# Kernel tuning notes

Measured on AMD Instinct MI355X. Metric: run time of the kernel, lower is better.

Reference implementation:

```python
import jax, jax.numpy as jnp
import numpy as np
import math

B, T, C = 2, 2048, 768
NH, HD = 12, 64  # n_head, head_dim

def setup_inputs() -> dict:
    key = jax.random.key(0)
    k1, k2, k3 = jax.random.split(key, 3)
    x = jax.random.normal(k1, (B, T, C), dtype=jnp.float32)
    mask = jnp.tril(jnp.ones((T, T), dtype=bool))[None, None]  # [1,1,T,T] causal
    Wqkv = jax.random.normal(k2, (C, 3 * C), dtype=jnp.float32) * (1.0 / math.sqrt(C))
    Wproj = jax.random.normal(k3, (C, C), dtype=jnp.float32) * (1.0 / math.sqrt(C))
    return {"x": x, "mask": mask, "Wqkv": Wqkv, "Wproj": Wproj}

def reference(x, mask, Wqkv, Wproj):
    b, t, c = x.shape
    qkv = x @ Wqkv  # [b,t,3c]
    q, k, v = jnp.split(qkv, 3, axis=-1)
    q = q.reshape(b, t, NH, HD).transpose(0, 2, 1, 3)  # [b,h,t,d]
    k = k.reshape(b, t, NH, HD).transpose(0, 2, 1, 3)
    v = v.reshape(b, t, NH, HD).transpose(0, 2, 1, 3)
    att = jnp.einsum('bhqd,bhkd->bhqk', q, k) / math.sqrt(HD)
    att = jnp.where(mask, att, -jnp.inf)
    att = jax.nn.softmax(att, axis=-1)
    out = jnp.einsum('bhqk,bhkd->bhqd', att, v)
    out = out.transpose(0, 2, 1, 3).reshape(b, t, c)
    return out @ Wproj
```

## Files before the change

### kernel.cpp

```cpp
#include <hip/hip_runtime.h>
#include <hip/hip_bf16.h>

#define T_   2048
#define C_   768
#define NH_  12
#define HD_  64
#define M_   (2*T_)
#define N1_  (3*C_)
#define PB_  ((size_t)NH_*T_*HD_)
#define KS_  0.180336880f

typedef __attribute__((ext_vector_type(8))) short  short8;
typedef __attribute__((ext_vector_type(4))) float  floatx4;

__device__ __forceinline__ floatx4 mfma_bf16(short8 a, short8 b, floatx4 c) {
    return __builtin_amdgcn_mfma_f32_16x16x32_bf16(a, b, c, 0, 0, 0);
}

__device__ __forceinline__ float fast_exp2(float x) {
    return __builtin_amdgcn_exp2f(x);
}

#define XSZ  3145728
#define WQSZ 1769472
#define WPSZ 589824
__global__ __launch_bounds__(256) void prep_cvt(const float* __restrict__ x,
                                                const float* __restrict__ wqkv,
                                                const float* __restrict__ wproj,
                                                __hip_bfloat16* __restrict__ xb,
                                                __hip_bfloat16* __restrict__ wqkvT,
                                                __hip_bfloat16* __restrict__ wprojT) {
    const int idx = blockIdx.x * 256 + threadIdx.x;
    if (idx < XSZ) {
        xb[idx] = __float2bfloat16(x[idx]);
    } else if (idx < XSZ + WQSZ) {
        const int j = idx - XSZ;
        const int n = j / C_, k = j - n * C_;
        wqkvT[j] = __float2bfloat16(wqkv[(size_t)k * N1_ + n]);
    } else {
        const int j = idx - XSZ - WQSZ;
        const int n = j / C_, k = j - n * C_;
        wprojT[j] = __float2bfloat16(wproj[(size_t)k * C_ + n]);
    }
}

__global__ __launch_bounds__(256) void gemm_bt(const __hip_bfloat16* __restrict__ A,
                                               const __hip_bfloat16* __restrict__ Bt,
                                               int N, int K, int mode,
                                               void* __restrict__ O0,
                                               __hip_bfloat16* __restrict__ O1,
                                               __hip_bfloat16* __restrict__ O2) {
    __shared__ __align__(16) __hip_bfloat16 As[64 * 40];
    __shared__ __align__(16) __hip_bfloat16 Bs[64 * 40];

    const int tid  = threadIdx.x;
    const int n0   = blockIdx.x * 64;
    const int m0   = blockIdx.y * 64;
    const int srow = tid >> 2;
    const int scol = (tid & 3) * 8;
    const int wave = tid >> 6;
    const int ln   = tid & 63;
    const int l16  = ln & 15;
    const int q4   = ln >> 4;
    const int wm   = (wave >> 1) * 32;
    const int wn   = (wave & 1) * 32;

    floatx4 acc[2][2];
#pragma unroll
    for (int i = 0; i < 2; i++)
#pragma unroll
        for (int j = 0; j < 2; j++) acc[i][j] = (floatx4){0.f, 0.f, 0.f, 0.f};

    const __hip_bfloat16* Ap = A  + (size_t)(m0 + srow) * K + scol;
    const __hip_bfloat16* Bp = Bt + (size_t)(n0 + srow) * K + scol;

    for (int k0 = 0; k0 < K; k0 += 32) {
        short8 av = *(const short8*)(Ap + k0);
        short8 bv = *(const short8*)(Bp + k0);
        __syncthreads();
        *(short8*)(As + srow * 40 + scol) = av;
        *(short8*)(Bs + srow * 40 + scol) = bv;
        __syncthreads();
        short8 af[2], bfr[2];
#pragma unroll
        for (int i = 0; i < 2; i++) {
            af[i]  = *(const short8*)(As + (wm + i * 16 + l16) * 40 + q4 * 8);
            bfr[i] = *(const short8*)(Bs + (wn + i * 16 + l16) * 40 + q4 * 8);
        }
#pragma unroll
        for (int i = 0; i < 2; i++)
#pragma unroll
            for (int j = 0; j < 2; j++)
                acc[i][j] = mfma_bf16(af[i], bfr[j], acc[i][j]);
    }

#pragma unroll
    for (int i = 0; i < 2; i++) {
        const int mbase = m0 + wm + i * 16 + q4 * 4;
#pragma unroll
        for (int j = 0; j < 2; j++) {
            const int n = n0 + wn + j * 16 + l16;
#pragma unroll
            for (int r = 0; r < 4; r++) {
                const int mm = mbase + r;
                const float fv = acc[i][j][r];
                if (mode == 1) {
                    ((float*)O0)[(size_t)mm * N + n] = fv;
                } else {
                    const __hip_bfloat16 hv = __float2bfloat16(fv);
                    const int which = n / C_;
                    const int rem   = n - which * C_;
                    const int h     = rem >> 6;
                    const int d     = rem & 63;
                    const int bh    = (mm >> 11) * NH_ + h;
                    const int t     = mm & (T_ - 1);
                    if (which == 0)      ((__hip_bfloat16*)O0)[((size_t)bh * T_ + t) * HD_ + d] = hv;
                    else if (which == 1) O1[((size_t)bh * T_ + t) * HD_ + d] = hv;
                    else                 O2[((size_t)bh * HD_ + d) * T_ + t] = hv;
                }
            }
        }
    }
}

__global__ __launch_bounds__(256) void gemm_xw(const void* __restrict__ A,
                                               const float* __restrict__ Bf,
                                               int a_is_f32, int row0, int N, int K,
                                               int mode, int orow0,
                                               void* __restrict__ O0,
                                               __hip_bfloat16* __restrict__ O1,
                                               __hip_bfloat16* __restrict__ O2) {
    __shared__ __align__(16) __hip_bfloat16 As[64 * 40];
    __shared__ __align__(16) __hip_bfloat16 Bs[64 * 40];

    const int tid  = threadIdx.x;
    const int n0   = blockIdx.x * 64;
    const int m0   = blockIdx.y * 64;
    const int srow = tid >> 2;
    const int scol = (tid & 3) * 8;
    const int wave = tid >> 6;
    const int ln   = tid & 63;
    const int l16  = ln & 15;
    const int q4   = ln >> 4;
    const int wm   = (wave >> 1) * 32;
    const int wn   = (wave & 1) * 32;

    floatx4 acc[2][2];
#pragma unroll
    for (int i = 0; i < 2; i++)
#pragma unroll
        for (int j = 0; j < 2; j++) acc[i][j] = (floatx4){0.f, 0.f, 0.f, 0.f};

    const size_t arow = (size_t)(row0 + m0 + srow) * K;

    for (int k0 = 0; k0 < K; k0 += 32) {
        union { __hip_bfloat16 h[8]; short8 v; } au, bu;
        if (a_is_f32) {
            const float* Af = (const float*)A;
            floatx4 f0 = *(const floatx4*)(Af + arow + k0 + scol);
            floatx4 f1 = *(const floatx4*)(Af + arow + k0 + scol + 4);
#pragma unroll
            for (int j = 0; j < 4; j++) {
                au.h[j]     = __float2bfloat16(f0[j]);
                au.h[4 + j] = __float2bfloat16(f1[j]);
            }
        } else {
            au.v = *(const short8*)((const __hip_bfloat16*)A + arow + k0 + scol);
        }
#pragma unroll
        for (int j = 0; j < 8; j++)
            bu.h[j] = __float2bfloat16(Bf[(size_t)(k0 + wave * 8 + j) * N + n0 + ln]);
        __syncthreads();
        *(short8*)(As + srow * 40 + scol) = au.v;
        *(short8*)(Bs + ln * 40 + wave * 8) = bu.v;
        __syncthreads();
        short8 af[2], bfr[2];
#pragma unroll
        for (int i = 0; i < 2; i++) {
            af[i]  = *(const short8*)(As + (wm + i * 16 + l16) * 40 + q4 * 8);
            bfr[i] = *(const short8*)(Bs + (wn + i * 16 + l16) * 40 + q4 * 8);
        }
#pragma unroll
        for (int i = 0; i < 2; i++)
#pragma unroll
            for (int j = 0; j < 2; j++)
                acc[i][j] = mfma_bf16(af[i], bfr[j], acc[i][j]);
    }

#pragma unroll
    for (int i = 0; i < 2; i++) {
        const int mbase = m0 + wm + i * 16 + q4 * 4;
#pragma unroll
        for (int j = 0; j < 2; j++) {
            const int n = n0 + wn + j * 16 + l16;
#pragma unroll
            for (int r = 0; r < 4; r++) {
                const int mm = mbase + r;
                const float fv = acc[i][j][r];
                if (mode == 1) {
                    ((float*)O0)[(size_t)(orow0 + mm) * N + n] = fv;
                } else {
                    const __hip_bfloat16 hv = __float2bfloat16(fv);
                    const int which = n / C_;
                    const int rem   = n - which * C_;
                    const int h     = rem >> 6;
                    const int d     = rem & 63;
                    const int bh    = (mm >> 11) * NH_ + h;
                    const int t     = mm & (T_ - 1);
                    if (which == 0)      ((__hip_bfloat16*)O0)[((size_t)bh * T_ + t) * HD_ + d] = hv;
                    else if (which == 1) O1[((size_t)bh * T_ + t) * HD_ + d] = hv;
                    else                 O2[((size_t)bh * HD_ + d) * T_ + t] = hv;
                }
            }
        }
    }
}

__global__ __launch_bounds__(128) void attn_fused(const __hip_bfloat16* __restrict__ Q,
                                                  const __hip_bfloat16* __restrict__ Kd,
                                                  const __hip_bfloat16* __restrict__ Vt,
                                                  __hip_bfloat16* __restrict__ O) {
    __shared__ __align__(16) __hip_bfloat16 plds[2][2][16][72];

    const int bh   = blockIdx.x;
    const int wid  = threadIdx.x >> 6;
    const int lane = threadIdx.x & 63;
    const int l16  = lane & 15;
    const int q4   = lane >> 4;
    const int i    = 63 - ((int)blockIdx.y * 2 + wid);
    const int q0A  = (2 * i) * 16;
    const int q0B  = (2 * i + 1) * 16;
    const int nch  = (i >> 1) + 1;

    const __hip_bfloat16* Qh = Q  + (size_t)bh * T_ * HD_;
    const __hip_bfloat16* Kh = Kd + (size_t)bh * T_ * HD_;
    const __hip_bfloat16* Vh = Vt + (size_t)bh * HD_ * T_;

    short8 aqA[2], aqB[2];
#pragma unroll
    for (int kt = 0; kt < 2; kt++) {
        aqA[kt] = *(const short8*)(Qh + (size_t)(q0A + l16) * HD_ + kt * 32 + q4 * 8);
        aqB[kt] = *(const short8*)(Qh + (size_t)(q0B + l16) * HD_ + kt * 32 + q4 * 8);
    }

    floatx4 accA[4], accB[4];
#pragma unroll
    for (int ct = 0; ct < 4; ct++) {
        accA[ct] = (floatx4){0.f, 0.f, 0.f, 0.f};
        accB[ct] = (floatx4){0.f, 0.f, 0.f, 0.f};
    }
    float mA[4], lA[4], mB[4], lB[4];
#pragma unroll
    for (int r = 0; r < 4; r++) { mA[r] = mB[r] = -3e38f; lA[r] = lB[r] = 0.f; }

    for (int c = 0; c < nch; ++c) {
        const int kv0 = c * 64;
        const bool diag = (c == nch - 1);

        short8 bk[4][2];
#pragma unroll
        for (int nt = 0; nt < 4; nt++)
#pragma unroll
            for (int kt = 0; kt < 2; kt++)
                bk[nt][kt] = *(const short8*)(Kh + (size_t)(kv0 + nt * 16 + l16) * HD_ + kt * 32 + q4 * 8);

        floatx4 sA[4], sB[4];
#pragma unroll
        for (int nt = 0; nt < 4; nt++) {
            sA[nt] = (floatx4){0.f, 0.f, 0.f, 0.f};
            sB[nt] = (floatx4){0.f, 0.f, 0.f, 0.f};
#pragma unroll
            for (int kt = 0; kt < 2; kt++) {
                sA[nt] = mfma_bf16(aqA[kt], bk[nt][kt], sA[nt]);
                sB[nt] = mfma_bf16(aqB[kt], bk[nt][kt], sB[nt]);
            }
        }

        if (diag) {
#pragma unroll
            for (int r = 0; r < 4; r++) {
#pragma unroll
                for (int nt = 0; nt < 4; nt++) {
                    const int kvc = kv0 + nt * 16 + l16;
                    if (kvc > q0A + q4 * 4 + r) sA[nt][r] = -3e38f;
                    if (kvc > q0B + q4 * 4 + r) sB[nt][r] = -3e38f;
                }
            }
        }

        float mxA[4], mxB[4];
#pragma unroll
        for (int r = 0; r < 4; r++) {
            mxA[r] = fmaxf(fmaxf(sA[0][r], sA[1][r]), fmaxf(sA[2][r], sA[3][r]));
            mxB[r] = fmaxf(fmaxf(sB[0][r], sB[1][r]), fmaxf(sB[2][r], sB[3][r]));
        }
#pragma unroll
        for (int off = 1; off < 16; off <<= 1)
#pragma unroll
            for (int r = 0; r < 4; r++) {
                mxA[r] = fmaxf(mxA[r], __shfl_xor(mxA[r], off, 64));
                mxB[r] = fmaxf(mxB[r], __shfl_xor(mxB[r], off, 64));
            }

        float rsA[4], rsB[4], alA[4], alB[4];
#pragma unroll
        for (int r = 0; r < 4; r++) {
            const float mnA = fmaxf(mA[r], mxA[r]);
            const float mnB = fmaxf(mB[r], mxB[r]);
            alA[r] = fast_exp2((mA[r] - mnA) * KS_);
            alB[r] = fast_exp2((mB[r] - mnB) * KS_);
            mA[r] = mnA; mB[r] = mnB;
            const float mkA = mnA * KS_, mkB = mnB * KS_;
            float ra = 0.f, rb = 0.f;
#pragma unroll
            for (int nt = 0; nt < 4; nt++) {
                const float pa = fast_exp2(sA[nt][r] * KS_ - mkA);
                const float pb = fast_exp2(sB[nt][r] * KS_ - mkB);
                plds[wid][0][q4 * 4 + r][nt * 16 + l16] = __float2bfloat16(pa);
                plds[wid][1][q4 * 4 + r][nt * 16 + l16] = __float2bfloat16(pb);
                ra += pa; rb += pb;
            }
            rsA[r] = ra; rsB[r] = rb;
        }
#pragma unroll
        for (int off = 1; off < 16; off <<= 1)
#pragma unroll
            for (int r = 0; r < 4; r++) {
                rsA[r] += __shfl_xor(rsA[r], off, 64);
                rsB[r] += __shfl_xor(rsB[r], off, 64);
            }
#pragma unroll
        for (int r = 0; r < 4; r++) {
            lA[r] = alA[r] * lA[r] + rsA[r];
            lB[r] = alB[r] * lB[r] + rsB[r];
        }
#pragma unroll
        for (int ct = 0; ct < 4; ct++)
#pragma unroll
            for (int r = 0; r < 4; r++) {
                accA[ct][r] *= alA[r];
                accB[ct][r] *= alB[r];
            }

        __threadfence_block();

        short8 apA[2], apB[2];
#pragma unroll
        for (int kt = 0; kt < 2; kt++) {
            apA[kt] = *(const short8*)(&plds[wid][0][l16][kt * 32 + q4 * 8]);
            apB[kt] = *(const short8*)(&plds[wid][1][l16][kt * 32 + q4 * 8]);
        }
#pragma unroll
        for (int ct = 0; ct < 4; ct++)
#pragma unroll
            for (int kt = 0; kt < 2; kt++) {
                short8 bv = *(const short8*)(Vh + (size_t)(ct * 16 + l16) * T_ + kv0 + kt * 32 + q4 * 8);
                accA[ct] = mfma_bf16(apA[kt], bv, accA[ct]);
                accB[ct] = mfma_bf16(apB[kt], bv, accB[ct]);
            }

        __threadfence_block();
    }

    const int orow0 = (bh / NH_) * T_;
    const int hcol  = (bh % NH_) * HD_;
#pragma unroll
    for (int r = 0; r < 4; r++) {
        const float invA = 1.0f / lA[r];
        const float invB = 1.0f / lB[r];
        __hip_bfloat16* oA = O + (size_t)(orow0 + q0A + q4 * 4 + r) * C_ + hcol;
        __hip_bfloat16* oB = O + (size_t)(orow0 + q0B + q4 * 4 + r) * C_ + hcol;
#pragma unroll
        for (int ct = 0; ct < 4; ct++) {
            oA[ct * 16 + l16] = __float2bfloat16(accA[ct][r] * invA);
            oB[ct * 16 + l16] = __float2bfloat16(accB[ct][r] * invB);
        }
    }
}

extern "C" void kernel_launch(void* const* d_in, const int* in_sizes, int n_in,
                              void* d_out, int out_size, void* d_ws, size_t ws_size,
                              hipStream_t stream) {
    const float *x = nullptr, *wqkv = nullptr, *wproj = nullptr;
    for (int i = 0; i < n_in; i++) {
        const int s = in_sizes[i];
        if (s == M_ * C_ && !x) x = (const float*)d_in[i];
        else if (s == C_ * N1_ && !wqkv) wqkv = (const float*)d_in[i];
        else if (s == C_ * C_ && !wproj) wproj = (const float*)d_in[i];
    }
    float* out = (float*)d_out;
    __hip_bfloat16* ws = (__hip_bfloat16*)d_ws;
    __hip_bfloat16* Vt = (__hip_bfloat16*)d_out;

    const size_t needA = (size_t)(XSZ + WQSZ + WPSZ + 3 * XSZ) * 2;
    const size_t needB = 6 * PB_ * 2;
    if (ws_size >= needA) {
        __hip_bfloat16* xb     = ws;
        __hip_bfloat16* wqkvT  = xb + XSZ;
        __hip_bfloat16* wprojT = wqkvT + WQSZ;
        __hip_bfloat16* Qall   = wprojT + WPSZ;
        __hip_bfloat16* Kall   = Qall + XSZ;
        __hip_bfloat16* ATT    = Kall + XSZ;
        prep_cvt<<<dim3((XSZ + WQSZ + WPSZ) / 256), 256, 0, stream>>>(x, wqkv, wproj, xb, wqkvT, wprojT);
        gemm_bt<<<dim3(N1_ / 64, M_ / 64), 256, 0, stream>>>(xb, wqkvT, N1_, C_, 0, (void*)Qall, Kall, Vt);
        attn_fused<<<dim3(2 * NH_, 32), 128, 0, stream>>>(Qall, Kall, Vt, ATT);
        gemm_bt<<<dim3(C_ / 64, M_ / 64), 256, 0, stream>>>(ATT, wprojT, C_, C_, 1, (void*)out, nullptr, nullptr);
    } else if (ws_size >= needB) {
        __hip_bfloat16* Qall = ws;
        __hip_bfloat16* Kall = Qall + 2 * PB_;
        __hip_bfloat16* ATT  = Kall + 2 * PB_;
        gemm_xw<<<dim3(N1_ / 64, M_ / 64), 256, 0, stream>>>(
            x, wqkv, 1, 0, N1_, C_, 0, 0, (void*)Qall, Kall, Vt);
        attn_fused<<<dim3(2 * NH_, 32), 128, 0, stream>>>(Qall, Kall, Vt, ATT);
        gemm_xw<<<dim3(C_ / 64, M_ / 64), 256, 0, stream>>>(
            ATT, wproj, 0, 0, C_, C_, 1, 0, (void*)out, nullptr, nullptr);
    } else {
        __hip_bfloat16* Qb      = ws;
        __hip_bfloat16* Kb      = Qb + PB_;
        __hip_bfloat16* ATTb[2] = {Kb + PB_, Kb + 2 * PB_};
        for (int b = 0; b < 2; b++) {
            __hip_bfloat16* Vtb = Vt + (size_t)b * PB_;
            gemm_xw<<<dim3(N1_ / 64, 32), 256, 0, stream>>>(
                x, wqkv, 1, b * T_, N1_, C_, 0, 0, (void*)Qb, Kb, Vtb);
            attn_fused<<<dim3(NH_, 32), 128, 0, stream>>>(Qb, Kb, Vtb, ATTb[b]);
        }
        for (int b = 0; b < 2; b++)
            gemm_xw<<<dim3(C_ / 64, 32), 256, 0, stream>>>(
                ATTb[b], wproj, 0, 0, C_, C_, 1, b * T_, (void*)out, nullptr, nullptr);
    }
}
```

Before: 238.5 us.

## Enlarge fused-convert GEMM tiles, split attention KV across waves, drop prep path

Removes the separate bf16 conversion/transpose kernel and the bf16-transposed GEMM path, so QKV and projection always use the on-the-fly fp32→bf16 GEMM, now with 128x128 tiles and 4x4 MFMA fragments per wave. The attention kernel now gives each block one 32-row query pair, with the two waves splitting the KV chunks between them and merging their partial softmax states through shared memory. This removes an extra kernel launch and its memory traffic and balances causal work across waves. In exchange it adds strided fp32 weight reads with in-loop conversion, fewer GEMM blocks (lower occupancy and parallelism), and a cross-wave reduction step.

Measured after the change: 212.9 us. 10.7% less time.

```diff
diff --git a/kernel.cpp b/kernel.cpp
--- a/kernel.cpp
+++ b/kernel.cpp
@@ -16,111 +16,8 @@
 __device__ __forceinline__ floatx4 mfma_bf16(short8 a, short8 b, floatx4 c) {
     return __builtin_amdgcn_mfma_f32_16x16x32_bf16(a, b, c, 0, 0, 0);
 }
-
 __device__ __forceinline__ float fast_exp2(float x) {
     return __builtin_amdgcn_exp2f(x);
-}
-
-#define XSZ  3145728
-#define WQSZ 1769472
-#define WPSZ 589824
-__global__ __launch_bounds__(256) void prep_cvt(const float* __restrict__ x,
-                                                const float* __restrict__ wqkv,
-                                                const float* __restrict__ wproj,
-                                                __hip_bfloat16* __restrict__ xb,
-                                                __hip_bfloat16* __restrict__ wqkvT,
-                                                __hip_bfloat16* __restrict__ wprojT) {
-    const int idx = blockIdx.x * 256 + threadIdx.x;
-    if (idx < XSZ) {
-        xb[idx] = __float2bfloat16(x[idx]);
-    } else if (idx < XSZ + WQSZ) {
-        const int j = idx - XSZ;
-        const int n = j / C_, k = j - n * C_;
-        wqkvT[j] = __float2bfloat16(wqkv[(size_t)k * N1_ + n]);
-    } else {
-        const int j = idx - XSZ - WQSZ;
-        const int n = j / C_, k = j - n * C_;
-        wprojT[j] = __float2bfloat16(wproj[(size_t)k * C_ + n]);
-    }
-}
-
-__global__ __launch_bounds__(256) void gemm_bt(const __hip_bfloat16* __restrict__ A,
-                                               const __hip_bfloat16* __restrict__ Bt,
-                                               int N, int K, int mode,
-                                               void* __restrict__ O0,
-                                               __hip_bfloat16* __restrict__ O1,
-                                               __hip_bfloat16* __restrict__ O2) {
-    __shared__ __align__(16) __hip_bfloat16 As[64 * 40];
-    __shared__ __align__(16) __hip_bfloat16 Bs[64 * 40];
-
-    const int tid  = threadIdx.x;
-    const int n0   = blockIdx.x * 64;
-    const int m0   = blockIdx.y * 64;
-    const int srow = tid >> 2;
-    const int scol = (tid & 3) * 8;
-    const int wave = tid >> 6;
-    const int ln   = tid & 63;
-    const int l16  = ln & 15;
-    const int q4   = ln >> 4;
-    const int wm   = (wave >> 1) * 32;
-    const int wn   = (wave & 1) * 32;
-
-    floatx4 acc[2][2];
-#pragma unroll
-    for (int i = 0; i < 2; i++)
-#pragma unroll
-        for (int j = 0; j < 2; j++) acc[i][j] = (floatx4){0.f, 0.f, 0.f, 0.f};
-
-    const __hip_bfloat16* Ap = A  + (size_t)(m0 + srow) * K + scol;
-    const __hip_bfloat16* Bp = Bt + (size_t)(n0 + srow) * K + scol;
-
-    for (int k0 = 0; k0 < K; k0 += 32) {
-        short8 av = *(const short8*)(Ap + k0);
-        short8 bv = *(const short8*)(Bp + k0);
-        __syncthreads();
-        *(short8*)(As + srow * 40 + scol) = av;
-        *(short8*)(Bs + srow * 40 + scol) = bv;
-        __syncthreads();
-        short8 af[2], bfr[2];
-#pragma unroll
-        for (int i = 0; i < 2; i++) {
-            af[i]  = *(const short8*)(As + (wm + i * 16 + l16) * 40 + q4 * 8);
-            bfr[i] = *(const short8*)(Bs + (wn + i * 16 + l16) * 40 + q4 * 8);
-        }
-#pragma unroll
-        for (int i = 0; i < 2; i++)
-#pragma unroll
-            for (int j = 0; j < 2; j++)
-                acc[i][j] = mfma_bf16(af[i], bfr[j], acc[i][j]);
-    }
-
-#pragma unroll
-    for (int i = 0; i < 2; i++) {
-        const int mbase = m0 + wm + i * 16 + q4 * 4;
-#pragma unroll
-        for (int j = 0; j < 2; j++) {
-            const int n = n0 + wn + j * 16 + l16;
-#pragma unroll
-            for (int r = 0; r < 4; r++) {
-                const int mm = mbase + r;
-                const float fv = acc[i][j][r];
-                if (mode == 1) {
-                    ((float*)O0)[(size_t)mm * N + n] = fv;
-                } else {
-                    const __hip_bfloat16 hv = __float2bfloat16(fv);
-                    const int which = n / C_;
-                    const int rem   = n - which * C_;
-                    const int h     = rem >> 6;
-                    const int d     = rem & 63;
-                    const int bh    = (mm >> 11) * NH_ + h;
-                    const int t     = mm & (T_ - 1);
-                    if (which == 0)      ((__hip_bfloat16*)O0)[((size_t)bh * T_ + t) * HD_ + d] = hv;
-                    else if (which == 1) O1[((size_t)bh * T_ + t) * HD_ + d] = hv;
-                    else                 O2[((size_t)bh * HD_ + d) * T_ + t] = hv;
-                }
-            }
-        }
-    }
 }
 
 __global__ __launch_bounds__(256) void gemm_xw(const void* __restrict__ A,
@@ -130,68 +27,79 @@
                                                void* __restrict__ O0,
                                                __hip_bfloat16* __restrict__ O1,
                                                __hip_bfloat16* __restrict__ O2) {
-    __shared__ __align__(16) __hip_bfloat16 As[64 * 40];
-    __shared__ __align__(16) __hip_bfloat16 Bs[64 * 40];
+    __shared__ __align__(16) __hip_bfloat16 As[128 * 40];
+    __shared__ __align__(16) __hip_bfloat16 Bs[128 * 40];
 
     const int tid  = threadIdx.x;
-    const int n0   = blockIdx.x * 64;
-    const int m0   = blockIdx.y * 64;
-    const int srow = tid >> 2;
-    const int scol = (tid & 3) * 8;
+    const int n0   = blockIdx.x * 128;
+    const int m0   = blockIdx.y * 128;
+    const int srow = tid >> 1;
+    const int scol = (tid & 1) * 16;
+    const int bn   = tid & 127;
+    const int bg   = tid >> 7;
     const int wave = tid >> 6;
     const int ln   = tid & 63;
     const int l16  = ln & 15;
     const int q4   = ln >> 4;
-    const int wm   = (wave >> 1) * 32;
-    const int wn   = (wave & 1) * 32;
-
-    floatx4 acc[2][2];
-#pragma unroll
-    for (int i = 0; i < 2; i++)
-#pragma unroll
-        for (int j = 0; j < 2; j++) acc[i][j] = (floatx4){0.f, 0.f, 0.f, 0.f};
+    const int wm   = (wave >> 1) * 64;
+    const int wn   = (wave & 1) * 64;
+
+    floatx4 acc[4][4];
+#pragma unroll
+    for (int i = 0; i < 4; i++)
+#pragma unroll
+        for (int j = 0; j < 4; j++) acc[i][j] = (floatx4){0.f, 0.f, 0.f, 0.f};
 
     const size_t arow = (size_t)(row0 + m0 + srow) * K;
 
     for (int k0 = 0; k0 < K; k0 += 32) {
-        union { __hip_bfloat16 h[8]; short8 v; } au, bu;
+        union { __hip_bfloat16 h[16]; short8 v[2]; } au, bu;
         if (a_is_f32) {
             const float* Af = (const float*)A;
-            floatx4 f0 = *(const floatx4*)(Af + arow + k0 + scol);
-            floatx4 f1 = *(const floatx4*)(Af + arow + k0 + scol + 4);
+            const size_t base = arow + k0 + scol;
+            floatx4 f0 = *(const floatx4*)(Af + base);
+            floatx4 f1 = *(const floatx4*)(Af + base + 4);
+            floatx4 f2 = *(const floatx4*)(Af + base + 8);
+            floatx4 f3 = *(const floatx4*)(Af + base + 12);
 #pragma unroll
             for (int j = 0; j < 4; j++) {
-                au.h[j]     = __float2bfloat16(f0[j]);
-                au.h[4 + j] = __float2bfloat16(f1[j]);
+                au.h[j]      = __float2bfloat16(f0[j]);
+                au.h[4 + j]  = __float2bfloat16(f1[j]);
+                au.h[8 + j]  = __float2bfloat16(f2[j]);
+                au.h[12 + j] = __float2bfloat16(f3[j]);
             }
         } else {
-            au.v = *(const short8*)((const __hip_bfloat16*)A + arow + k0 + scol);
-        }
-#pragma unroll
-        for (int j = 0; j < 8; j++)
-            bu.h[j] = __float2bfloat16(Bf[(size_t)(k0 + wave * 8 + j) * N + n0 + ln]);
+            const __hip_bfloat16* Ab = (const __hip_bfloat16*)A;
+            au.v[0] = *(const short8*)(Ab + arow + k0 + scol);
+            au.v[1] = *(const short8*)(Ab + arow + k0 + scol + 8);
+        }
+#pragma unroll
+        for (int j = 0; j < 16; j++)
+            bu.h[j] = __float2bfloat16(Bf[(size_t)(k0 + bg * 16 + j) * N + n0 + bn]);
         __syncthreads();
-        *(short8*)(As + srow * 40 + scol) = au.v;
-        *(short8*)(Bs + ln * 40 + wave * 8) = bu.v;
+        *(short8*)(As + srow * 40 + scol)     = au.v[0];
+        *(short8*)(As + srow * 40 + scol + 8) = au.v[1];
+        *(short8*)(Bs + bn * 40 + bg * 16)     = bu.v[0];
+        *(short8*)(Bs + bn * 40 + bg * 16 + 8) = bu.v[1];
         __syncthreads();
-        short8 af[2], bfr[2];
-#pragma unroll
-        for (int i = 0; i < 2; i++) {
+        short8 af[4], bfr[4];
+#pragma unroll
+        for (int i = 0; i < 4; i++) {
             af[i]  = *(const short8*)(As + (wm + i * 16 + l16) * 40 + q4 * 8);
             bfr[i] = *(const short8*)(Bs + (wn + i * 16 + l16) * 40 + q4 * 8);
         }
 #pragma unroll
-        for (int i = 0; i < 2; i++)
-#pragma unroll
-            for (int j = 0; j < 2; j++)
+        for (int i = 0; i < 4; i++)
+#pragma unroll
+            for (int j = 0; j < 4; j++)
                 acc[i][j] = mfma_bf16(af[i], bfr[j], acc[i][j]);
     }
 
 #pragma unroll
-    for (int i = 0; i < 2; i++) {
+    for (int i = 0; i < 4; i++) {
         const int mbase = m0 + wm + i * 16 + q4 * 4;
 #pragma unroll
-        for (int j = 0; j < 2; j++) {
+        for (int j = 0; j < 4; j++) {
             const int n = n0 + wn + j * 16 + l16;
 #pragma unroll
             for (int r = 0; r < 4; r++) {
@@ -221,15 +129,17 @@
                                                   const __hip_bfloat16* __restrict__ Vt,
                                                   __hip_bfloat16* __restrict__ O) {
     __shared__ __align__(16) __hip_bfloat16 plds[2][2][16][72];
+    __shared__ __align__(16) floatx4 accbuf[2][4][64];
+    __shared__ float mbuf[2][16], lbuf[2][16];
 
     const int bh   = blockIdx.x;
     const int wid  = threadIdx.x >> 6;
     const int lane = threadIdx.x & 63;
     const int l16  = lane & 15;
     const int q4   = lane >> 4;
-    const int i    = 63 - ((int)blockIdx.y * 2 + wid);
-    const int q0A  = (2 * i) * 16;
-    const int q0B  = (2 * i + 1) * 16;
+    const int i    = 63 - (int)blockIdx.y;
+    const int q0A  = 32 * i;
+    const int q0B  = 32 * i + 16;
     const int nch  = (i >> 1) + 1;
 
     const __hip_bfloat16* Qh = Q  + (size_t)bh * T_ * HD_;
@@ -253,7 +163,7 @@
 #pragma unroll
     for (int r = 0; r < 4; r++) { mA[r] = mB[r] = -3e38f; lA[r] = lB[r] = 0.f; }
 
-    for (int c = 0; c < nch; ++c) {
+    for (int c = wid; c < nch; c += 2) {
         const int kv0 = c * 64;
         const bool diag = (c == nch - 1);
 
@@ -362,18 +272,42 @@
         __threadfence_block();
     }
 
+    __syncthreads();
+    if (wid == 0) {
+        if (l16 == 0)
+#pragma unroll
+            for (int r = 0; r < 4; r++) { mbuf[1][q4 * 4 + r] = mB[r]; lbuf[1][q4 * 4 + r] = lB[r]; }
+#pragma unroll
+        for (int ct = 0; ct < 4; ct++) accbuf[1][ct][lane] = accB[ct];
+    } else {
+        if (l16 == 0)
+#pragma unroll
+            for (int r = 0; r < 4; r++) { mbuf[0][q4 * 4 + r] = mA[r]; lbuf[0][q4 * 4 + r] = lA[r]; }
+#pragma unroll
+        for (int ct = 0; ct < 4; ct++) accbuf[0][ct][lane] = accA[ct];
+    }
+    __syncthreads();
+
     const int orow0 = (bh / NH_) * T_;
     const int hcol  = (bh % NH_) * HD_;
+    const int slot  = wid;
+    const int q0    = wid ? q0B : q0A;
 #pragma unroll
     for (int r = 0; r < 4; r++) {
-        const float invA = 1.0f / lA[r];
-        const float invB = 1.0f / lB[r];
-        __hip_bfloat16* oA = O + (size_t)(orow0 + q0A + q4 * 4 + r) * C_ + hcol;
-        __hip_bfloat16* oB = O + (size_t)(orow0 + q0B + q4 * 4 + r) * C_ + hcol;
+        const float m0v = wid ? mB[r] : mA[r];
+        const float l0v = wid ? lB[r] : lA[r];
+        const float m1v = mbuf[slot][q4 * 4 + r];
+        const float l1v = lbuf[slot][q4 * 4 + r];
+        const float ms  = fmaxf(m0v, m1v);
+        const float w0  = fast_exp2((m0v - ms) * KS_);
+        const float w1  = fast_exp2((m1v - ms) * KS_);
+        const float inv = 1.0f / (l0v * w0 + l1v * w1);
+        __hip_bfloat16* orow = O + (size_t)(orow0 + q0 + q4 * 4 + r) * C_ + hcol;
 #pragma unroll
         for (int ct = 0; ct < 4; ct++) {
-            oA[ct * 16 + l16] = __float2bfloat16(accA[ct][r] * invA);
-            oB[ct * 16 + l16] = __float2bfloat16(accB[ct][r] * invB);
+            const float a0 = wid ? accB[ct][r] : accA[ct][r];
+            const float a1 = accbuf[slot][ct][lane][r];
+            orow[ct * 16 + l16] = __float2bfloat16((a0 * w0 + a1 * w1) * inv);
         }
     }
 }
@@ -392,27 +326,15 @@
     __hip_bfloat16* ws = (__hip_bfloat16*)d_ws;
     __hip_bfloat16* Vt = (__hip_bfloat16*)d_out;
 
-    const size_t needA = (size_t)(XSZ + WQSZ + WPSZ + 3 * XSZ) * 2;
     const size_t needB = 6 * PB_ * 2;
-    if (ws_size >= needA) {
-        __hip_bfloat16* xb     = ws;
-        __hip_bfloat16* wqkvT  = xb + XSZ;
-        __hip_bfloat16* wprojT = wqkvT + WQSZ;
-        __hip_bfloat16* Qall   = wprojT + WPSZ;
-        __hip_bfloat16* Kall   = Qall + XSZ;
-        __hip_bfloat16* ATT    = Kall + XSZ;
-        prep_cvt<<<dim3((XSZ + WQSZ + WPSZ) / 256), 256, 0, stream>>>(x, wqkv, wproj, xb, wqkvT, wprojT);
-        gemm_bt<<<dim3(N1_ / 64, M_ / 64), 256, 0, stream>>>(xb, wqkvT, N1_, C_, 0, (void*)Qall, Kall, Vt);
-        attn_fused<<<dim3(2 * NH_, 32), 128, 0, stream>>>(Qall, Kall, Vt, ATT);
-        gemm_bt<<<dim3(C_ / 64, M_ / 64), 256, 0, stream>>>(ATT, wprojT, C_, C_, 1, (void*)out, nullptr, nullptr);
-    } else if (ws_size >= needB) {
+    if (ws_size >= needB) {
         __hip_bfloat16* Qall = ws;
         __hip_bfloat16* Kall = Qall + 2 * PB_;
         __hip_bfloat16* ATT  = Kall + 2 * PB_;
-        gemm_xw<<<dim3(N1_ / 64, M_ / 64), 256, 0, stream>>>(
+        gemm_xw<<<dim3(N1_ / 128, M_ / 128), 256, 0, stream>>>(
             x, wqkv, 1, 0, N1_, C_, 0, 0, (void*)Qall, Kall, Vt);
-        attn_fused<<<dim3(2 * NH_, 32), 128, 0, stream>>>(Qall, Kall, Vt, ATT);
-        gemm_xw<<<dim3(C_ / 64, M_ / 64), 256, 0, stream>>>(
+        attn_fused<<<dim3(2 * NH_, 64), 128, 0, stream>>>(Qall, Kall, Vt, ATT);
+        gemm_xw<<<dim3(C_ / 128, M_ / 128), 256, 0, stream>>>(
             ATT, wproj, 0, 0, C_, C_, 1, 0, (void*)out, nullptr, nullptr);
     } else {
         __hip_bfloat16* Qb      = ws;
@@ -420,12 +342,12 @@
         __hip_bfloat16* ATTb[2] = {Kb + PB_, Kb + 2 * PB_};
         for (int b = 0; b < 2; b++) {
             __hip_bfloat16* Vtb = Vt + (size_t)b * PB_;
-            gemm_xw<<<dim3(N1_ / 64, 32), 256, 0, stream>>>(
+            gemm_xw<<<dim3(N1_ / 128, T_ / 128), 256, 0, stream>>>(
                 x, wqkv, 1, b * T_, N1_, C_, 0, 0, (void*)Qb, Kb, Vtb);
-            attn_fused<<<dim3(NH_, 32), 128, 0, stream>>>(Qb, Kb, Vtb, ATTb[b]);
+            attn_fused<<<dim3(NH_, 64), 128, 0, stream>>>(Qb, Kb, Vtb, ATTb[b]);
         }
         for (int b = 0; b < 2; b++)
-            gemm_xw<<<dim3(C_ / 64, 32), 256, 0, stream>>>(
+            gemm_xw<<<dim3(C_ / 128, T_ / 128), 256, 0, stream>>>(
                 ATTb[b], wproj, 0, 0, C_, C_, 1, b * T_, (void*)out, nullptr, nullptr);
     }
 }
```
